# Performance work log

Measured on AMD Instinct MI355X. Metric: run time of the kernel, lower is better.

## Reference

```python
import jax, jax.numpy as jnp
import numpy as np


def setup_inputs() -> dict:
    key = jax.random.key(0)
    k0, k1, k2, k3 = jax.random.split(key, 4)
    B, S, D, F, E = 2, 2048, 1024, 4096, 8
    scale = 0.02
    return {
        "x": jax.random.normal(k0, (B, S, D), jnp.float32),
        "gate_w": jax.random.normal(k1, (E, D), jnp.float32) * scale,
        "gate_b": jnp.zeros((E,), jnp.float32),
        "w1": jax.random.normal(k2, (E, D, F), jnp.float32) * scale,
        "b1": jnp.zeros((E, F), jnp.float32),
        "w2": jax.random.normal(k3, (E, F, D), jnp.float32) * scale,
        "b2": jnp.zeros((E, D), jnp.float32),
        "top_k": 2,
    }


def reference(x, gate_w, gate_b, w1, b1, w2, b2, top_k):
    B, S, D = x.shape
    E = gate_w.shape[0]
    xt = x.reshape(-1, D)                                   # [T, D]
    T = xt.shape[0]

    # Router: softmax over gate logits, then top-k and renormalize.
    gate_probs = jax.nn.softmax(xt @ gate_w.T + gate_b, axis=-1)   # [T, E]
    weights, selected = jax.lax.top_k(gate_probs, top_k)           # [T, k]
    weights = weights / jnp.sum(weights, axis=-1, keepdims=True)

    # Per-token combine weights over experts (zero where not selected),
    # equivalent to the per-expert gather/scatter loop in the original.
    combine = jnp.zeros((T, E), x.dtype).at[
        jnp.arange(T)[:, None], selected
    ].add(weights)                                                 # [T, E]

    # Expert MLPs (dense over experts, masked combine).
    h = jax.nn.silu(jnp.einsum("td,edf->etf", xt, w1) + b1[:, None, :])  # [E, T, F]
    expert_out = jnp.einsum("etf,efd->etd", h, w2) + b2[:, None, :]      # [E, T, D]
    out = jnp.einsum("etd,te->td", expert_out, combine)                  # [T, D]
    return out.reshape(B, S, D)
```

## Files before the change

### kernel.cpp

```cpp
#include <hip/hip_runtime.h>

#define T_TOK 4096
#define DIM   1024
#define FDIM  4096
#define NEXP  8

typedef __bf16 bf16x8 __attribute__((ext_vector_type(8)));
typedef __bf16 bf16x4 __attribute__((ext_vector_type(4)));
typedef float  f32x4  __attribute__((ext_vector_type(4)));

__device__ __forceinline__ void glds16(const void* g, void* l) {
    __builtin_amdgcn_global_load_lds(
        (const __attribute__((address_space(1))) void*)g,
        (__attribute__((address_space(3))) void*)l, 16, 0, 0);
}

__device__ __forceinline__ int xcd_swz(int phys, int total) {
    int q = total >> 3, r = total & 7;
    int x = phys & 7, i = phys >> 3;
    return (x < r ? x * (q + 1) : r * (q + 1) + (x - r) * q) + i;
}

__global__ __launch_bounds__(64)
void moe_router(const float* __restrict__ x,
                const float* __restrict__ gw,
                const float* __restrict__ gb,
                const int*   __restrict__ topk_p,
                int*   __restrict__ counts,
                int*   __restrict__ bucket,
                float* __restrict__ bweight,
                __bf16* __restrict__ xb) {
    const int t = blockIdx.x;
    const int lane = threadIdx.x;
    float part[NEXP];
#pragma unroll
    for (int e = 0; e < NEXP; ++e) part[e] = 0.f;
    const float* xrow = x + (size_t)t * DIM;
    __bf16* xbrow = xb + (size_t)t * DIM;
#pragma unroll
    for (int r = 0; r < 4; ++r) {
        int c = r * 256 + lane * 4;
        float4 v = *(const float4*)&xrow[c];
        bf16x4 o; o[0]=(__bf16)v.x; o[1]=(__bf16)v.y; o[2]=(__bf16)v.z; o[3]=(__bf16)v.w;
        *(bf16x4*)&xbrow[c] = o;
#pragma unroll
        for (int e = 0; e < NEXP; ++e) {
            float4 g = *(const float4*)&gw[e * DIM + c];
            part[e] += v.x*g.x + v.y*g.y + v.z*g.z + v.w*g.w;
        }
    }
#pragma unroll
    for (int off = 32; off > 0; off >>= 1) {
#pragma unroll
        for (int e = 0; e < NEXP; ++e) part[e] += __shfl_xor(part[e], off);
    }
    if (lane == 0) {
        int k = topk_p[0];
        if (k < 1) k = 1;
        if (k > NEXP) k = NEXP;
        float p[NEXP];
        float mx = -1e30f;
#pragma unroll
        for (int e = 0; e < NEXP; ++e) {
            p[e] = part[e] + gb[e];
            mx = fmaxf(mx, p[e]);
        }
#pragma unroll
        for (int e = 0; e < NEXP; ++e) p[e] = __expf(p[e] - mx);
        bool used[NEXP];
#pragma unroll
        for (int e = 0; e < NEXP; ++e) used[e] = false;
        int sel[NEXP]; float selp[NEXP]; float wsum = 0.f;
        for (int j = 0; j < k; ++j) {
            int best = 0; float bv = -1.f;
            for (int e = 0; e < NEXP; ++e)
                if (!used[e] && p[e] > bv) { bv = p[e]; best = e; }
            used[best] = true; sel[j] = best; selp[j] = bv; wsum += bv;
        }
        for (int j = 0; j < k; ++j) {
            int e = sel[j];
            int pos = atomicAdd(&counts[e], 1);
            bucket[e * T_TOK + pos]  = t;
            bweight[e * T_TOK + pos] = selp[j] / wsum;
        }
    }
}

__global__ __launch_bounds__(256)
void transpose_cvt(const float* __restrict__ in, __bf16* __restrict__ out,
                   int R, int C) {
    const size_t zo = (size_t)blockIdx.z * R * C;
    in += zo; out += zo;
    __shared__ float ts[64][129];
    const int r0 = blockIdx.x * 128, c0 = blockIdx.y * 64;
    const int t = threadIdx.x;
    const int rr = t >> 4;
    const int cl = (t & 15) * 4;
    float4 v[8];
#pragma unroll
    for (int p = 0; p < 8; ++p)
        v[p] = *(const float4*)&in[(size_t)(r0 + p * 16 + rr) * C + c0 + cl];
#pragma unroll
    for (int p = 0; p < 8; ++p) {
        ts[cl + 0][p * 16 + rr] = v[p].x;
        ts[cl + 1][p * 16 + rr] = v[p].y;
        ts[cl + 2][p * 16 + rr] = v[p].z;
        ts[cl + 3][p * 16 + rr] = v[p].w;
    }
    __syncthreads();
    const int oc = t >> 4;
    const int orc = (t & 15) * 8;
#pragma unroll
    for (int p = 0; p < 4; ++p) {
        bf16x8 o;
#pragma unroll
        for (int j = 0; j < 8; ++j) o[j] = (__bf16)ts[p * 16 + oc][orc + j];
        *(bf16x8*)&out[(size_t)(c0 + p * 16 + oc) * R + r0 + orc] = o;
    }
}

__global__ __launch_bounds__(64)
void build_work(const int* __restrict__ counts, int* __restrict__ hdr) {
    __shared__ int off1[NEXP + 1];
    const int lane = threadIdx.x;
    if (lane == 0) {
        int a = 0;
        for (int e = 0; e < NEXP; ++e) {
            off1[e] = a;
            a += (counts[e] + 127) >> 7;
        }
        off1[NEXP] = a;
        hdr[0] = a;
    }
    __syncthreads();
    for (int e = 0; e < NEXP; ++e) {
        int n1 = off1[e + 1] - off1[e];
        for (int j = lane; j < n1; j += 64) hdr[8 + off1[e] + j] = (e << 16) | j;
    }
}


__global__ __launch_bounds__(256, 4)
void moe_gemm1(const __bf16* __restrict__ xb,
               const __bf16* __restrict__ w1t,
               const float*  __restrict__ b1,
               const int*    __restrict__ counts,
               const int*    __restrict__ bucket,
               const int*    __restrict__ hdr,
               __bf16* __restrict__ H) {
    __shared__ __bf16 smem[16384];
    __shared__ int tok_s[128];
    const int tid = threadIdx.x;
    const int wave = tid >> 6, lane = tid & 63;
    const int wm = wave & 1, wn = wave >> 1;
    const int quad = lane >> 4, l15 = lane & 15;
    const int lrow = lane >> 2;
    const int lk8  = (lane & 3) * 8;
    char* sb = (char*)smem;
    char* dA0 = sb + wave * 2048;
    char* dA1 = sb + 8192 + wave * 2048;
    char* dB0 = sb + 16384 + wave * 2048;
    char* dB1 = sb + 24576 + wave * 2048;

    const int n1 = hdr[0];
    const int total = n1 * (FDIM / 128);
    for (int phys = blockIdx.x; phys < total; phys += gridDim.x) {
        const int u = xcd_swz(phys, total);
        const int entry = hdr[8 + (u % n1)];
        const int e = entry >> 16, tile = entry & 0xffff;
        const int nb = (u / n1) * 128;
        const int cnt = counts[e];
        if (tid < 128) {
            int r = tile * 128 + tid;
            if (r >= cnt) r = cnt - 1;
            tok_s[tid] = bucket[e * T_TOK + r];
        }
        __syncthreads();

        const int ar0 = wave * 32 + lrow;
        const __bf16* pA0 = xb + (size_t)tok_s[ar0]      * DIM + lk8;
        const __bf16* pA1 = xb + (size_t)tok_s[ar0 + 16] * DIM + lk8;
        const __bf16* pB0 = w1t + ((size_t)e * FDIM + nb + wave * 32 + lrow) * DIM + lk8;
        const __bf16* pB1 = pB0 + (size_t)16 * DIM;

        f32x4 acc[4][4];
#pragma unroll
        for (int i = 0; i < 4; ++i)
#pragma unroll
            for (int j = 0; j < 4; ++j) acc[i][j] = (f32x4){0.f,0.f,0.f,0.f};

        for (int k0 = 0; k0 < DIM; k0 += 64) {
            glds16(pA0 + k0,      dA0);
            glds16(pA0 + k0 + 32, dA1);
            glds16(pA1 + k0,      dA0 + 1024);
            glds16(pA1 + k0 + 32, dA1 + 1024);
            glds16(pB0 + k0,      dB0);
            glds16(pB0 + k0 + 32, dB1);
            glds16(pB1 + k0,      dB0 + 1024);
            glds16(pB1 + k0 + 32, dB1 + 1024);
            __syncthreads();
#pragma unroll
            for (int kk = 0; kk < 2; ++kk) {
                bf16x8 af[4], bfr[4];
#pragma unroll
                for (int i = 0; i < 4; ++i)
                    af[i] = *(const bf16x8*)&smem[kk*4096 + (wm*64 + i*16 + l15)*32 + quad*8];
#pragma unroll
                for (int j = 0; j < 4; ++j)
                    bfr[j] = *(const bf16x8*)&smem[8192 + kk*4096 + (wn*64 + j*16 + l15)*32 + quad*8];
#pragma unroll
                for (int i = 0; i < 4; ++i)
#pragma unroll
                    for (int j = 0; j < 4; ++j)
                        acc[i][j] = __builtin_amdgcn_mfma_f32_16x16x32_bf16(
                            af[i], bfr[j], acc[i][j], 0, 0, 0);
            }
            __syncthreads();
        }

        __bf16* stg = (__bf16*)(sb + wave * 2304);
        const float* b1e = b1 + e * FDIM + nb + wn * 64;
#pragma unroll
        for (int i = 0; i < 4; ++i) {
#pragma unroll
            for (int j = 0; j < 4; ++j) {
                float bias = b1e[j * 16 + l15];
#pragma unroll
                for (int r = 0; r < 4; ++r) {
                    float v = acc[i][j][r] + bias;
                    float s = v / (1.f + __expf(-v));
                    stg[(quad*4 + r) * 72 + j*16 + l15] = (__bf16)s;
                }
            }
            int prow = tile * 128 + wm * 64 + i * 16 + lrow;
            if (prow < cnt) {
                bf16x8 v0 = *(const bf16x8*)&stg[lrow * 72 + (lane & 3) * 16];
                bf16x8 v1 = *(const bf16x8*)&stg[lrow * 72 + (lane & 3) * 16 + 8];
                __bf16* dst = H + (size_t)(e * T_TOK + prow) * FDIM
                              + nb + wn * 64 + (lane & 3) * 16;
                *(bf16x8*)dst = v0;
                *(bf16x8*)(dst + 8) = v1;
            }
        }
        __syncthreads();
    }
}

#define KSPLIT 2
#define KHALF  (FDIM / KSPLIT)

__global__ __launch_bounds__(256, 4)
void moe_gemm2(const __bf16* __restrict__ H,
               const __bf16* __restrict__ w2t,
               const float*  __restrict__ b2,
               const int*    __restrict__ counts,
               const int*    __restrict__ bucket,
               const float*  __restrict__ bweight,
               const int*    __restrict__ hdr,
               float* __restrict__ out) {
    __shared__ __bf16 smem[16384];
    __shared__ int   tok_s[128];
    __shared__ float w_s[128];
    const int tid = threadIdx.x;
    const int wave = tid >> 6, lane = tid & 63;
    const int wm = wave & 1, wn = wave >> 1;
    const int quad = lane >> 4, l15 = lane & 15;
    const int lrow = lane >> 2;
    const int lk8  = (lane & 3) * 8;
    char* sb = (char*)smem;
    char* dA0 = sb + wave * 2048;
    char* dA1 = sb + 8192 + wave * 2048;
    char* dB0 = sb + 16384 + wave * 2048;
    char* dB1 = sb + 24576 + wave * 2048;

    const int n1 = hdr[0];
    const int total = n1 * (DIM / 128) * KSPLIT;
    for (int phys = blockIdx.x; phys < total; phys += gridDim.x) {
        const int u = xcd_swz(phys, total);
        const int entry = hdr[8 + (u % n1)];
        const int e = entry >> 16, tile = entry & 0xffff;
        const int rest = u / n1;
        const int nb = (rest & 7) * 128;
        const int kc = rest >> 3;
        const int cnt = counts[e];
        if (tid < 128) {
            int r  = tile * 128 + tid;
            int rc = r < cnt ? r : cnt - 1;
            tok_s[tid] = bucket[e * T_TOK + rc];
            w_s[tid]   = bweight[e * T_TOK + rc];
        }
        __syncthreads();

        const size_t kbase = (size_t)kc * KHALF;
        const __bf16* pA0 = H + (size_t)(e * T_TOK + tile * 128 + wave * 32 + lrow) * FDIM
                              + kbase + lk8;
        const __bf16* pA1 = pA0 + (size_t)16 * FDIM;
        const __bf16* pB0 = w2t + ((size_t)e * DIM + nb + wave * 32 + lrow) * FDIM
                              + kbase + lk8;
        const __bf16* pB1 = pB0 + (size_t)16 * FDIM;

        f32x4 acc[4][4];
#pragma unroll
        for (int i = 0; i < 4; ++i)
#pragma unroll
            for (int j = 0; j < 4; ++j) acc[i][j] = (f32x4){0.f,0.f,0.f,0.f};

        for (int k0 = 0; k0 < KHALF; k0 += 64) {
            glds16(pA0 + k0,      dA0);
            glds16(pA0 + k0 + 32, dA1);
            glds16(pA1 + k0,      dA0 + 1024);
            glds16(pA1 + k0 + 32, dA1 + 1024);
            glds16(pB0 + k0,      dB0);
            glds16(pB0 + k0 + 32, dB1);
            glds16(pB1 + k0,      dB0 + 1024);
            glds16(pB1 + k0 + 32, dB1 + 1024);
            __syncthreads();
#pragma unroll
            for (int kk = 0; kk < 2; ++kk) {
                bf16x8 af[4], bfr[4];
#pragma unroll
                for (int i = 0; i < 4; ++i)
                    af[i] = *(const bf16x8*)&smem[kk*4096 + (wm*64 + i*16 + l15)*32 + quad*8];
#pragma unroll
                for (int j = 0; j < 4; ++j)
                    bfr[j] = *(const bf16x8*)&smem[8192 + kk*4096 + (wn*64 + j*16 + l15)*32 + quad*8];
#pragma unroll
                for (int i = 0; i < 4; ++i)
#pragma unroll
                    for (int j = 0; j < 4; ++j)
                        acc[i][j] = __builtin_amdgcn_mfma_f32_16x16x32_bf16(
                            af[i], bfr[j], acc[i][j], 0, 0, 0);
            }
            __syncthreads();
        }

#pragma unroll
        for (int i = 0; i < 4; ++i)
#pragma unroll
            for (int j = 0; j < 4; ++j)
#pragma unroll
                for (int r = 0; r < 4; ++r) {
                    int m = wm*64 + i*16 + quad*4 + r;
                    int prow = tile * 128 + m;
                    if (prow < cnt) {
                        int dc = nb + wn*64 + j*16 + l15;
                        float v = acc[i][j][r] + (kc == 0 ? b2[e * DIM + dc] : 0.f);
                        atomicAdd(&out[(size_t)tok_s[m] * DIM + dc], w_s[m] * v);
                    }
                }
        __syncthreads();
    }
}

extern "C" void kernel_launch(void* const* d_in, const int* in_sizes, int n_in,
                              void* d_out, int out_size, void* d_ws, size_t ws_size,
                              hipStream_t stream) {
    const float* x  = (const float*)d_in[0];
    const float* gw = (const float*)d_in[1];
    const float* gb = (const float*)d_in[2];
    const float* w1 = (const float*)d_in[3];
    const float* b1 = (const float*)d_in[4];
    const float* w2 = (const float*)d_in[5];
    const float* b2 = (const float*)d_in[6];
    const int* topk = (const int*)d_in[7];
    float* out = (float*)d_out;

    char* ws = (char*)d_ws;
    size_t off = 0;
    int* counts = (int*)(ws + off);    off += 256;
    int* bucket = (int*)(ws + off);    off += (size_t)NEXP * T_TOK * 4;
    float* bw   = (float*)(ws + off);  off += (size_t)NEXP * T_TOK * 4;
    int* hdr    = (int*)(ws + off);    off += 4096;
    off = (off + 255) & ~(size_t)255;
    __bf16* xb  = (__bf16*)(ws + off); off += (size_t)T_TOK * DIM * 2;
    __bf16* w1t = (__bf16*)(ws + off); off += (size_t)NEXP * DIM * FDIM * 2;
    __bf16* w2t = (__bf16*)(ws + off); off += (size_t)NEXP * FDIM * DIM * 2;
    __bf16* H   = (__bf16*)(ws + off);

    hipMemsetAsync(counts, 0, 256, stream);
    hipMemsetAsync(out, 0, (size_t)out_size * 4, stream);

    moe_router<<<T_TOK, 64, 0, stream>>>(x, gw, gb, topk, counts, bucket, bw, xb);
    transpose_cvt<<<dim3(DIM/128, FDIM/64, NEXP), 256, 0, stream>>>(w1, w1t, DIM, FDIM);
    transpose_cvt<<<dim3(FDIM/128, DIM/64, NEXP), 256, 0, stream>>>(w2, w2t, FDIM, DIM);
    build_work<<<1, 64, 0, stream>>>(counts, hdr);

    moe_gemm1<<<2048, 256, 0, stream>>>(xb, w1t, b1, counts, bucket, hdr, H);
    moe_gemm2<<<1024, 256, 0, stream>>>(H, w2t, b2, counts, bucket, bw, hdr, out);
}
```

Baseline: 724.5 us.

## Double-buffer LDS k-tiles in both MoE GEMMs with inline-asm ds_reads

```diff
diff --git a/kernel.cpp b/kernel.cpp
--- a/kernel.cpp
+++ b/kernel.cpp
@@ -8,12 +8,16 @@
 typedef __bf16 bf16x8 __attribute__((ext_vector_type(8)));
 typedef __bf16 bf16x4 __attribute__((ext_vector_type(4)));
 typedef float  f32x4  __attribute__((ext_vector_type(4)));
+typedef const __attribute__((address_space(3))) char* lds3;
 
 __device__ __forceinline__ void glds16(const void* g, void* l) {
     __builtin_amdgcn_global_load_lds(
         (const __attribute__((address_space(1))) void*)g,
         (__attribute__((address_space(3))) void*)l, 16, 0, 0);
 }
+
+#define DSR(dst, a, imm) \
+    asm volatile("ds_read_b128 %0, %1 offset:" #imm : "=v"(dst) : "v"(a))
 
 __device__ __forceinline__ int xcd_swz(int phys, int total) {
     int q = total >> 3, r = total & 7;
@@ -139,6 +143,54 @@
     }
 }
 
+#define STAGE(DST, KO) do { \
+    glds16(pA0 + (KO), (DST)); \
+    glds16(pA1 + (KO), (DST) + 1024); \
+    glds16(pB0 + (KO), (DST) + 8192); \
+    glds16(pB1 + (KO), (DST) + 9216); } while (0)
+
+#define PHASE(APTR, BPTR) do { \
+    bf16x8 af[4], bfr[4]; \
+    DSR(af[0], (APTR), 0);    DSR(af[1], (APTR), 1024); \
+    DSR(af[2], (APTR), 2048); DSR(af[3], (APTR), 3072); \
+    DSR(bfr[0], (BPTR), 0);    DSR(bfr[1], (BPTR), 1024); \
+    DSR(bfr[2], (BPTR), 2048); DSR(bfr[3], (BPTR), 3072); \
+    asm volatile("s_waitcnt lgkmcnt(0)"); \
+    __builtin_amdgcn_sched_barrier(0); \
+    __builtin_amdgcn_s_setprio(1); \
+    _Pragma("unroll") for (int i_ = 0; i_ < 4; ++i_) \
+    _Pragma("unroll") for (int j_ = 0; j_ < 4; ++j_) \
+        acc[i_][j_] = __builtin_amdgcn_mfma_f32_16x16x32_bf16( \
+            af[i_], bfr[j_], acc[i_][j_], 0, 0, 0); \
+    __builtin_amdgcn_s_setprio(0); \
+    __builtin_amdgcn_sched_barrier(0); \
+    __syncthreads(); } while (0)
+
+#define KLOOP2(NT) do { \
+    STAGE(stg0, 0); \
+    __syncthreads(); \
+    _Pragma("unroll 1") \
+    for (int t_ = 0; t_ < (NT); t_ += 2) { \
+        STAGE(stg1, (t_ + 1) * 32); \
+        PHASE(aP0, bP0); \
+        if (t_ + 2 < (NT)) STAGE(stg0, (t_ + 2) * 32); \
+        PHASE(aP1, bP1); \
+    } } while (0)
+
+#define GEMM_LANES \
+    const int tid = threadIdx.x; \
+    const int wave = tid >> 6, lane = tid & 63; \
+    const int wm = wave & 1, wn = wave >> 1; \
+    const int quad = lane >> 4, l15 = lane & 15; \
+    const int lrow = lane >> 2; \
+    const int lk8  = (lane & 3) * 8; \
+    char* stg0 = sb + wave * 2048; \
+    char* stg1 = stg0 + 16384; \
+    lds3 s3 = (lds3)sb; \
+    lds3 aP0 = s3 + (wm * 64 + l15) * 64 + quad * 16; \
+    lds3 bP0 = s3 + 8192 + (wn * 64 + l15) * 64 + quad * 16; \
+    lds3 aP1 = aP0 + 16384; \
+    lds3 bP1 = bP0 + 16384;
 
 __global__ __launch_bounds__(256, 4)
 void moe_gemm1(const __bf16* __restrict__ xb,
@@ -148,19 +200,9 @@
                const int*    __restrict__ bucket,
                const int*    __restrict__ hdr,
                __bf16* __restrict__ H) {
-    __shared__ __bf16 smem[16384];
+    __shared__ __align__(16) char sb[32768];
     __shared__ int tok_s[128];
-    const int tid = threadIdx.x;
-    const int wave = tid >> 6, lane = tid & 63;
-    const int wm = wave & 1, wn = wave >> 1;
-    const int quad = lane >> 4, l15 = lane & 15;
-    const int lrow = lane >> 2;
-    const int lk8  = (lane & 3) * 8;
-    char* sb = (char*)smem;
-    char* dA0 = sb + wave * 2048;
-    char* dA1 = sb + 8192 + wave * 2048;
-    char* dB0 = sb + 16384 + wave * 2048;
-    char* dB1 = sb + 24576 + wave * 2048;
+    GEMM_LANES
 
     const int n1 = hdr[0];
     const int total = n1 * (FDIM / 128);
@@ -189,34 +231,7 @@
 #pragma unroll
             for (int j = 0; j < 4; ++j) acc[i][j] = (f32x4){0.f,0.f,0.f,0.f};
 
-        for (int k0 = 0; k0 < DIM; k0 += 64) {
-            glds16(pA0 + k0,      dA0);
-            glds16(pA0 + k0 + 32, dA1);
-            glds16(pA1 + k0,      dA0 + 1024);
-            glds16(pA1 + k0 + 32, dA1 + 1024);
-            glds16(pB0 + k0,      dB0);
-            glds16(pB0 + k0 + 32, dB1);
-            glds16(pB1 + k0,      dB0 + 1024);
-            glds16(pB1 + k0 + 32, dB1 + 1024);
-            __syncthreads();
-#pragma unroll
-            for (int kk = 0; kk < 2; ++kk) {
-                bf16x8 af[4], bfr[4];
-#pragma unroll
-                for (int i = 0; i < 4; ++i)
-                    af[i] = *(const bf16x8*)&smem[kk*4096 + (wm*64 + i*16 + l15)*32 + quad*8];
-#pragma unroll
-                for (int j = 0; j < 4; ++j)
-                    bfr[j] = *(const bf16x8*)&smem[8192 + kk*4096 + (wn*64 + j*16 + l15)*32 + quad*8];
-#pragma unroll
-                for (int i = 0; i < 4; ++i)
-#pragma unroll
-                    for (int j = 0; j < 4; ++j)
-                        acc[i][j] = __builtin_amdgcn_mfma_f32_16x16x32_bf16(
-                            af[i], bfr[j], acc[i][j], 0, 0, 0);
-            }
-            __syncthreads();
-        }
+        KLOOP2(DIM / 32);
 
         __bf16* stg = (__bf16*)(sb + wave * 2304);
         const float* b1e = b1 + e * FDIM + nb + wn * 64;
@@ -258,20 +273,10 @@
                const float*  __restrict__ bweight,
                const int*    __restrict__ hdr,
                float* __restrict__ out) {
-    __shared__ __bf16 smem[16384];
+    __shared__ __align__(16) char sb[32768];
     __shared__ int   tok_s[128];
     __shared__ float w_s[128];
-    const int tid = threadIdx.x;
-    const int wave = tid >> 6, lane = tid & 63;
-    const int wm = wave & 1, wn = wave >> 1;
-    const int quad = lane >> 4, l15 = lane & 15;
-    const int lrow = lane >> 2;
-    const int lk8  = (lane & 3) * 8;
-    char* sb = (char*)smem;
-    char* dA0 = sb + wave * 2048;
-    char* dA1 = sb + 8192 + wave * 2048;
-    char* dB0 = sb + 16384 + wave * 2048;
-    char* dB1 = sb + 24576 + wave * 2048;
+    GEMM_LANES
 
     const int n1 = hdr[0];
     const int total = n1 * (DIM / 128) * KSPLIT;
@@ -305,34 +310,7 @@
 #pragma unroll
             for (int j = 0; j < 4; ++j) acc[i][j] = (f32x4){0.f,0.f,0.f,0.f};
 
-        for (int k0 = 0; k0 < KHALF; k0 += 64) {
-            glds16(pA0 + k0,      dA0);
-            glds16(pA0 + k0 + 32, dA1);
-            glds16(pA1 + k0,      dA0 + 1024);
-            glds16(pA1 + k0 + 32, dA1 + 1024);
-            glds16(pB0 + k0,      dB0);
-            glds16(pB0 + k0 + 32, dB1);
-            glds16(pB1 + k0,      dB0 + 1024);
-            glds16(pB1 + k0 + 32, dB1 + 1024);
-            __syncthreads();
-#pragma unroll
-            for (int kk = 0; kk < 2; ++kk) {
-                bf16x8 af[4], bfr[4];
-#pragma unroll
-                for (int i = 0; i < 4; ++i)
-                    af[i] = *(const bf16x8*)&smem[kk*4096 + (wm*64 + i*16 + l15)*32 + quad*8];
-#pragma unroll
-                for (int j = 0; j < 4; ++j)
-                    bfr[j] = *(const bf16x8*)&smem[8192 + kk*4096 + (wn*64 + j*16 + l15)*32 + quad*8];
-#pragma unroll
-                for (int i = 0; i < 4; ++i)
-#pragma unroll
-                    for (int j = 0; j < 4; ++j)
-                        acc[i][j] = __builtin_amdgcn_mfma_f32_16x16x32_bf16(
-                            af[i], bfr[j], acc[i][j], 0, 0, 0);
-            }
-            __syncthreads();
-        }
+        KLOOP2(KHALF / 32);
 
 #pragma unroll
         for (int i = 0; i < 4; ++i)
```

Measured after the change: 720.6 us. Within noise of the previous version (-0.5%).
